# Performance work log

Hardware: AMD Instinct MI355X
Metric: run time of the kernel (lower is better)

The kernel has to match this reference:

```python
import jax, jax.numpy as jnp
import numpy as np

T, B, D_IN, H = 512, 64, 512, 1024


def setup_inputs() -> dict:
    key = jax.random.key(0)
    ks = jax.random.split(key, 6)
    s = 1.0 / np.sqrt(D_IN + H)  # torch Linear default init scale
    return {
        "x": jax.random.normal(ks[0], (T, B, D_IN), jnp.float32),
        "h0": jnp.zeros((B, H), jnp.float32),
        "C0": jnp.zeros((B, H), jnp.float32),
        "W_in": jax.random.normal(ks[1], (D_IN + H, H), jnp.float32) * s,
        "b_in": jnp.zeros((H,), jnp.float32),
        "W_over": jax.random.normal(ks[2], (D_IN + H, H), jnp.float32) * s,
        "b_over": jnp.zeros((H,), jnp.float32),
        "W_out": jax.random.normal(ks[3], (D_IN + H, H), jnp.float32) * s,
        "b_out": jnp.zeros((H,), jnp.float32),
        "W_intern": jax.random.normal(ks[4], (D_IN + H, H), jnp.float32) * s,
        "b_intern": jnp.zeros((H,), jnp.float32),
    }


def reference(x, h0, C0, W_in, b_in, W_over, b_over, W_out, b_out, W_intern, b_intern):
    # Faithful translation: concat order is (h, x) per one_step.
    def step(carry, xt):
        h, C = carry
        xc = jnp.concatenate([h, xt], axis=1)               # [B, H + D_IN]
        to_keep = jax.nn.sigmoid(xc @ W_in + b_in)          # input gate
        to_throw = jax.nn.sigmoid(xc @ W_over + b_over)     # forget gate
        out = jax.nn.sigmoid(xc @ W_out + b_out)            # output gate
        Ct = to_throw * C + to_keep * jnp.tanh(xc @ W_intern + b_intern)
        ht = out * jnp.tanh(Ct)
        return (ht, Ct), ht

    (hT, CT), hs = jax.lax.scan(step, (h0, C0), x)
    return hs, CT  # ([T, B, H], [B, H])
```

## Files before the change

### kernel.cpp

```cpp
#include <hip/hip_runtime.h>
#include <hip/hip_bf16.h>
#include <stdint.h>

#define T_STEPS 512
#define BATCH   64
#define DIN     512
#define HID     1024
#define KDIM    1536
#define NBLK    128
#define HPB     8
#define GCPB    32
#define KGRPS   192

typedef __bf16 bf16x8 __attribute__((ext_vector_type(8)));
typedef float  f32x4  __attribute__((ext_vector_type(4)));
typedef unsigned short ushort_t;
typedef unsigned long long u64_t;

__device__ __forceinline__ ushort_t f2bf(float f) {
    union { float f; unsigned u; } v; v.f = f;
    unsigned u = v.u;
    u += 0x7FFFu + ((u >> 16) & 1u);
    return (ushort_t)(u >> 16);
}

__device__ __forceinline__ float fast_sig(float x) {
    return __builtin_amdgcn_rcpf(1.0f + __expf(-x));
}
__device__ __forceinline__ float fast_tanh(float x) {
    float e = __expf(2.0f * x);
    return 1.0f - 2.0f * __builtin_amdgcn_rcpf(e + 1.0f);
}

__global__ void cvt_x(const float* __restrict__ x, ushort_t* __restrict__ xb, int n8) {
    int i = blockIdx.x * blockDim.x + threadIdx.x;
    if (i >= n8) return;
    float4 v0 = ((const float4*)x)[2 * i];
    float4 v1 = ((const float4*)x)[2 * i + 1];
    uint4 o;
    o.x = (unsigned)f2bf(v0.x) | ((unsigned)f2bf(v0.y) << 16);
    o.y = (unsigned)f2bf(v0.z) | ((unsigned)f2bf(v0.w) << 16);
    o.z = (unsigned)f2bf(v1.x) | ((unsigned)f2bf(v1.y) << 16);
    o.w = (unsigned)f2bf(v1.z) | ((unsigned)f2bf(v1.w) << 16);
    ((uint4*)xb)[i] = o;
}

__global__ void xpose_w(const float* __restrict__ Wi, const float* __restrict__ Wf,
                        const float* __restrict__ Wo, const float* __restrict__ Wg,
                        ushort_t* __restrict__ wt) {
    __shared__ float tile[64][65];
    int kt = blockIdx.x, nt = blockIdx.y, g = blockIdx.z;
    const float* W = (g == 0) ? Wi : (g == 1) ? Wf : (g == 2) ? Wo : Wg;
    int k0 = kt * 64, n0 = nt * 64;
    int c = threadIdx.x & 63, r0 = threadIdx.x >> 6;
#pragma unroll
    for (int i = 0; i < 16; ++i) {
        int r = r0 + i * 4;
        tile[r][c] = W[(size_t)(k0 + r) * HID + n0 + c];
    }
    __syncthreads();
#pragma unroll
    for (int p = 0; p < 2; ++p) {
        int q = threadIdx.x + p * 256;
        int n_inner = q & 7;
        int kgl = (q >> 3) & 7;
        int bl = q >> 6;
        int n = n0 + bl * 8 + n_inner;
        int blk = n >> 3;
        int nn = g * 8 + (n & 7);
        int kgrp = (k0 >> 3) + kgl;
        __align__(16) ushort_t tmp[8];
#pragma unroll
        for (int j = 0; j < 8; ++j) tmp[j] = f2bf(tile[kgl * 8 + j][bl * 8 + n_inner]);
        *(uint4*)(wt + ((((size_t)blk * KGRPS + kgrp) * GCPB + nn) << 3)) = *(const uint4*)tmp;
    }
}

__global__ __launch_bounds__(256, 1) void lstm_persist(
    const ushort_t* __restrict__ xbf,
    const ushort_t* __restrict__ wt,
    const float* __restrict__ h0, const float* __restrict__ C0,
    const float* __restrict__ b_i, const float* __restrict__ b_f,
    const float* __restrict__ b_o, const float* __restrict__ b_g,
    ushort_t* __restrict__ hbuf,
    unsigned* __restrict__ flags,
    float* __restrict__ out)
{
    __shared__ float gbuf[4][BATCH][GCPB + 2];
    __shared__ float Cl[BATCH][HPB + 1];
    __shared__ float biasl[GCPB];

    const int tid  = threadIdx.x;
    const int blk  = blockIdx.x;
    const int wave = tid >> 6;
    const int lane = tid & 63;
    const int j0   = blk * HPB;
    const int m_lane = lane & 15;
    const int quad   = lane >> 4;
    const int koff   = quad * 8;

    const ushort_t* wblk = wt + (size_t)blk * KGRPS * GCPB * 8;
    bf16x8 wbx[4][2], wbh[8][2];
#pragma unroll
    for (int cc = 0; cc < 4; ++cc) {
        const int kgrp = (32 + wave * 4 + cc) * 4 + quad;
        wbx[cc][0] = *(const bf16x8*)(wblk + ((size_t)kgrp * GCPB + m_lane) * 8);
        wbx[cc][1] = *(const bf16x8*)(wblk + ((size_t)kgrp * GCPB + 16 + m_lane) * 8);
    }
#pragma unroll
    for (int cc = 0; cc < 8; ++cc) {
        const int kgrp = (wave * 8 + cc) * 4 + quad;
        wbh[cc][0] = *(const bf16x8*)(wblk + ((size_t)kgrp * GCPB + m_lane) * 8);
        wbh[cc][1] = *(const bf16x8*)(wblk + ((size_t)kgrp * GCPB + 16 + m_lane) * 8);
    }

    if (tid < GCPB) {
        int g = tid >> 3, j = tid & 7;
        const float* bp = (g == 0) ? b_i : (g == 1) ? b_f : (g == 2) ? b_o : b_g;
        biasl[tid] = bp[j0 + j];
    }
    if (tid < 128) {
        int b = tid >> 1, jh = (tid & 1) * 4;
#pragma unroll
        for (int jj = 0; jj < 4; ++jj)
            Cl[b][jh + jj] = C0[b * HID + j0 + jh + jj];
        u64_t pk = 0;
#pragma unroll
        for (int jj = 0; jj < 4; ++jj)
            pk |= (u64_t)f2bf(h0[b * HID + j0 + jh + jj]) << (16 * jj);
        __hip_atomic_store((u64_t*)(hbuf + b * HID + j0 + jh), pk,
                           __ATOMIC_RELAXED, __HIP_MEMORY_SCOPE_AGENT);
    }
    asm volatile("s_waitcnt vmcnt(0)" ::: "memory");
    __syncthreads();
    if (tid == 0)
        __hip_atomic_store(&flags[blk * 32], 1u, __ATOMIC_RELAXED, __HIP_MEMORY_SCOPE_AGENT);

    int pb = 0;
    for (int t = 0; t < T_STEPS; ++t) {
        const ushort_t* xsrc = xbf + (size_t)t * BATCH * DIN;
        const ushort_t* hsrc = hbuf + pb * BATCH * HID;

        f32x4 acc[4][2];
#pragma unroll
        for (int rt = 0; rt < 4; ++rt)
#pragma unroll
            for (int ct = 0; ct < 2; ++ct)
                acc[rt][ct] = (f32x4){0.f, 0.f, 0.f, 0.f};

        bf16x8 ax[4][4];
#pragma unroll
        for (int cc = 0; cc < 4; ++cc) {
            const ushort_t* ap = xsrc + (wave * 4 + cc) * 32 + koff;
#pragma unroll
            for (int rt = 0; rt < 4; ++rt)
                ax[cc][rt] = *(const bf16x8*)(ap + (size_t)(rt * 16 + m_lane) * DIN);
        }
        __builtin_amdgcn_sched_barrier(0);

        if (tid < NBLK) {
            while (__hip_atomic_load(&flags[tid * 32], __ATOMIC_RELAXED,
                                     __HIP_MEMORY_SCOPE_AGENT) < (unsigned)(t + 1))
                __builtin_amdgcn_s_sleep(1);
        }
        __syncthreads();
        __builtin_amdgcn_fence(__ATOMIC_ACQUIRE, "agent");

        bf16x8 ah[8][4];
#pragma unroll
        for (int cc = 0; cc < 8; ++cc) {
            const ushort_t* ap = hsrc + (wave * 8 + cc) * 32 + koff;
#pragma unroll
            for (int rt = 0; rt < 4; ++rt)
                ah[cc][rt] = *(const bf16x8*)(ap + (size_t)(rt * 16 + m_lane) * HID);
        }
        __builtin_amdgcn_sched_barrier(0);

        asm volatile("" ::
            "v"(ax[0][0]), "v"(ax[0][1]), "v"(ax[0][2]), "v"(ax[0][3]),
            "v"(ax[1][0]), "v"(ax[1][1]), "v"(ax[1][2]), "v"(ax[1][3]),
            "v"(ax[2][0]), "v"(ax[2][1]), "v"(ax[2][2]), "v"(ax[2][3]),
            "v"(ax[3][0]), "v"(ax[3][1]), "v"(ax[3][2]), "v"(ax[3][3]));
#pragma unroll
        for (int cc = 0; cc < 4; ++cc)
#pragma unroll
            for (int rt = 0; rt < 4; ++rt) {
                acc[rt][0] = __builtin_amdgcn_mfma_f32_16x16x32_bf16(ax[cc][rt], wbx[cc][0], acc[rt][0], 0, 0, 0);
                acc[rt][1] = __builtin_amdgcn_mfma_f32_16x16x32_bf16(ax[cc][rt], wbx[cc][1], acc[rt][1], 0, 0, 0);
            }

        asm volatile("" ::
            "v"(ah[0][0]), "v"(ah[0][1]), "v"(ah[0][2]), "v"(ah[0][3]),
            "v"(ah[1][0]), "v"(ah[1][1]), "v"(ah[1][2]), "v"(ah[1][3]),
            "v"(ah[2][0]), "v"(ah[2][1]), "v"(ah[2][2]), "v"(ah[2][3]),
            "v"(ah[3][0]), "v"(ah[3][1]), "v"(ah[3][2]), "v"(ah[3][3]));
        asm volatile("" ::
            "v"(ah[4][0]), "v"(ah[4][1]), "v"(ah[4][2]), "v"(ah[4][3]),
            "v"(ah[5][0]), "v"(ah[5][1]), "v"(ah[5][2]), "v"(ah[5][3]),
            "v"(ah[6][0]), "v"(ah[6][1]), "v"(ah[6][2]), "v"(ah[6][3]),
            "v"(ah[7][0]), "v"(ah[7][1]), "v"(ah[7][2]), "v"(ah[7][3]));

#pragma unroll
        for (int cc = 0; cc < 8; ++cc)
#pragma unroll
            for (int rt = 0; rt < 4; ++rt) {
                acc[rt][0] = __builtin_amdgcn_mfma_f32_16x16x32_bf16(ah[cc][rt], wbh[cc][0], acc[rt][0], 0, 0, 0);
                acc[rt][1] = __builtin_amdgcn_mfma_f32_16x16x32_bf16(ah[cc][rt], wbh[cc][1], acc[rt][1], 0, 0, 0);
            }

#pragma unroll
        for (int rt = 0; rt < 4; ++rt)
#pragma unroll
            for (int ct = 0; ct < 2; ++ct)
#pragma unroll
                for (int r = 0; r < 4; ++r)
                    gbuf[wave][rt * 16 + quad * 4 + r][ct * 16 + m_lane] = acc[rt][ct][r];
        __syncthreads();

        float hv[4], cv[4];
        int b = tid >> 1, jh = (tid & 1) * 4;
        if (tid < 128) {
#pragma unroll
            for (int jj = 0; jj < 4; ++jj) {
                int j = jh + jj;
                float pre[4];
#pragma unroll
                for (int g = 0; g < 4; ++g) {
                    int col = g * 8 + j;
                    pre[g] = biasl[col] + gbuf[0][b][col] + gbuf[1][b][col]
                                        + gbuf[2][b][col] + gbuf[3][b][col];
                }
                float ig = fast_sig(pre[0]);
                float fg = fast_sig(pre[1]);
                float og = fast_sig(pre[2]);
                float gg = fast_tanh(pre[3]);
                float c_new = fg * Cl[b][jh + jj] + ig * gg;
                Cl[b][jh + jj] = c_new;
                cv[jj] = c_new;
                hv[jj] = og * fast_tanh(c_new);
            }
            u64_t pk = (u64_t)f2bf(hv[0]) | ((u64_t)f2bf(hv[1]) << 16)
                     | ((u64_t)f2bf(hv[2]) << 32) | ((u64_t)f2bf(hv[3]) << 48);
            __hip_atomic_store((u64_t*)(hbuf + (1 - pb) * BATCH * HID + b * HID + j0 + jh),
                               pk, __ATOMIC_RELAXED, __HIP_MEMORY_SCOPE_AGENT);
        }
        asm volatile("s_waitcnt vmcnt(0)" ::: "memory");
        __syncthreads();
        if (tid == 0)
            __hip_atomic_store(&flags[blk * 32], (unsigned)(t + 2), __ATOMIC_RELAXED,
                               __HIP_MEMORY_SCOPE_AGENT);

        if (tid < 128) {
            float4 o4; o4.x = hv[0]; o4.y = hv[1]; o4.z = hv[2]; o4.w = hv[3];
            *(float4*)(out + (size_t)t * BATCH * HID + b * HID + j0 + jh) = o4;
            if (t == T_STEPS - 1) {
                float4 c4; c4.x = cv[0]; c4.y = cv[1]; c4.z = cv[2]; c4.w = cv[3];
                *(float4*)(out + (size_t)T_STEPS * BATCH * HID + b * HID + j0 + jh) = c4;
            }
        }
        pb ^= 1;
    }
}

extern "C" void kernel_launch(void* const* d_in, const int* in_sizes, int n_in,
                              void* d_out, int out_size, void* d_ws, size_t ws_size,
                              hipStream_t stream) {
    (void)in_sizes; (void)n_in; (void)out_size; (void)ws_size;
    const float* x  = (const float*)d_in[0];
    const float* h0 = (const float*)d_in[1];
    const float* C0 = (const float*)d_in[2];
    const float* Wi = (const float*)d_in[3];
    const float* bi = (const float*)d_in[4];
    const float* Wf = (const float*)d_in[5];
    const float* bf = (const float*)d_in[6];
    const float* Wo = (const float*)d_in[7];
    const float* bo = (const float*)d_in[8];
    const float* Wg = (const float*)d_in[9];
    const float* bg = (const float*)d_in[10];
    float* out = (float*)d_out;

    char* ws = (char*)d_ws;
    unsigned*  flags = (unsigned*)ws;
    ushort_t*  hbuf  = (ushort_t*)(ws + 16384);
    ushort_t*  xb    = (ushort_t*)(ws + 16384 + 262144);
    ushort_t*  wt    = (ushort_t*)(ws + 16384 + 262144 + 33554432);

    hipMemsetAsync(flags, 0, 16384, stream);
    cvt_x<<<8192, 256, 0, stream>>>(x, xb, (T_STEPS * BATCH * DIN) / 8);
    xpose_w<<<dim3(24, 16, 4), 256, 0, stream>>>(Wi, Wf, Wo, Wg, wt);
    lstm_persist<<<NBLK, 256, 0, stream>>>(xb, wt, h0, C0, bi, bf, bo, bg, hbuf, flags, out);
}
```

Measured before the change: 5.381 ms.

## Halve persistent blocks to 64, widen per-block hidden slice, stage x-weights in LDS

The persistent LSTM kernel now runs 64 blocks, each owning 16 hidden units (64 gate columns) instead of 8, so fewer blocks take part in the per-step flag barrier. The recurrent-weight slice still lives in registers, now twice as wide. The input-weight slice has moved into a shared-memory buffer and is read back each step. All 256 threads now run the gate epilogue. The aim is to cut cross-block synchronisation and polling cost, in exchange for twice the MFMA work per block and extra LDS reads on the critical path.

Result: faster. 4.790 ms (-11.0%).

```diff
diff --git a/kernel.cpp b/kernel.cpp
--- a/kernel.cpp
+++ b/kernel.cpp
@@ -7,10 +7,11 @@
 #define DIN     512
 #define HID     1024
 #define KDIM    1536
-#define NBLK    128
-#define HPB     8
-#define GCPB    32
+#define NBLK    64
+#define HPB     16
+#define GCPB    64
 #define KGRPS   192
+#define XKG     64
 
 typedef __bf16 bf16x8 __attribute__((ext_vector_type(8)));
 typedef float  f32x4  __attribute__((ext_vector_type(4)));
@@ -66,8 +67,8 @@
         int kgl = (q >> 3) & 7;
         int bl = q >> 6;
         int n = n0 + bl * 8 + n_inner;
-        int blk = n >> 3;
-        int nn = g * 8 + (n & 7);
+        int blk = n >> 4;
+        int nn = g * HPB + (n & 15);
         int kgrp = (k0 >> 3) + kgl;
         __align__(16) ushort_t tmp[8];
 #pragma unroll
@@ -86,6 +87,7 @@
     unsigned* __restrict__ flags,
     float* __restrict__ out)
 {
+    __shared__ __align__(16) ushort_t Wlx[XKG][GCPB][8];
     __shared__ float gbuf[4][BATCH][GCPB + 2];
     __shared__ float Cl[BATCH][HPB + 1];
     __shared__ float biasl[GCPB];
@@ -100,27 +102,28 @@
     const int koff   = quad * 8;
 
     const ushort_t* wblk = wt + (size_t)blk * KGRPS * GCPB * 8;
-    bf16x8 wbx[4][2], wbh[8][2];
-#pragma unroll
-    for (int cc = 0; cc < 4; ++cc) {
-        const int kgrp = (32 + wave * 4 + cc) * 4 + quad;
-        wbx[cc][0] = *(const bf16x8*)(wblk + ((size_t)kgrp * GCPB + m_lane) * 8);
-        wbx[cc][1] = *(const bf16x8*)(wblk + ((size_t)kgrp * GCPB + 16 + m_lane) * 8);
-    }
+
+    bf16x8 wbh[8][4];
 #pragma unroll
     for (int cc = 0; cc < 8; ++cc) {
         const int kgrp = (wave * 8 + cc) * 4 + quad;
-        wbh[cc][0] = *(const bf16x8*)(wblk + ((size_t)kgrp * GCPB + m_lane) * 8);
-        wbh[cc][1] = *(const bf16x8*)(wblk + ((size_t)kgrp * GCPB + 16 + m_lane) * 8);
+#pragma unroll
+        for (int ct = 0; ct < 4; ++ct)
+            wbh[cc][ct] = *(const bf16x8*)(wblk + ((size_t)kgrp * GCPB + ct * 16 + m_lane) * 8);
+    }
+    {
+        const uint4* src = (const uint4*)(wblk + (size_t)128 * GCPB * 8);
+        uint4* dst = (uint4*)(&Wlx[0][0][0]);
+        for (int i = tid; i < XKG * GCPB; i += 256) dst[i] = src[i];
     }
 
     if (tid < GCPB) {
-        int g = tid >> 3, j = tid & 7;
+        int g = tid >> 4, j = tid & 15;
         const float* bp = (g == 0) ? b_i : (g == 1) ? b_f : (g == 2) ? b_o : b_g;
         biasl[tid] = bp[j0 + j];
     }
-    if (tid < 128) {
-        int b = tid >> 1, jh = (tid & 1) * 4;
+    {
+        int b = tid >> 2, jh = (tid & 3) * 4;
 #pragma unroll
         for (int jj = 0; jj < 4; ++jj)
             Cl[b][jh + jj] = C0[b * HID + j0 + jh + jj];
@@ -141,11 +144,11 @@
         const ushort_t* xsrc = xbf + (size_t)t * BATCH * DIN;
         const ushort_t* hsrc = hbuf + pb * BATCH * HID;
 
-        f32x4 acc[4][2];
+        f32x4 acc[4][4];
 #pragma unroll
         for (int rt = 0; rt < 4; ++rt)
 #pragma unroll
-            for (int ct = 0; ct < 2; ++ct)
+            for (int ct = 0; ct < 4; ++ct)
                 acc[rt][ct] = (f32x4){0.f, 0.f, 0.f, 0.f};
 
         bf16x8 ax[4][4];
@@ -165,6 +168,7 @@
         }
         __syncthreads();
         __builtin_amdgcn_fence(__ATOMIC_ACQUIRE, "agent");
+        __builtin_amdgcn_sched_barrier(0);
 
         bf16x8 ah[8][4];
 #pragma unroll
@@ -176,81 +180,69 @@
         }
         __builtin_amdgcn_sched_barrier(0);
 
-        asm volatile("" ::
-            "v"(ax[0][0]), "v"(ax[0][1]), "v"(ax[0][2]), "v"(ax[0][3]),
-            "v"(ax[1][0]), "v"(ax[1][1]), "v"(ax[1][2]), "v"(ax[1][3]),
-            "v"(ax[2][0]), "v"(ax[2][1]), "v"(ax[2][2]), "v"(ax[2][3]),
-            "v"(ax[3][0]), "v"(ax[3][1]), "v"(ax[3][2]), "v"(ax[3][3]));
-#pragma unroll
-        for (int cc = 0; cc < 4; ++cc)
-#pragma unroll
-            for (int rt = 0; rt < 4; ++rt) {
-                acc[rt][0] = __builtin_amdgcn_mfma_f32_16x16x32_bf16(ax[cc][rt], wbx[cc][0], acc[rt][0], 0, 0, 0);
-                acc[rt][1] = __builtin_amdgcn_mfma_f32_16x16x32_bf16(ax[cc][rt], wbx[cc][1], acc[rt][1], 0, 0, 0);
-            }
-
-        asm volatile("" ::
-            "v"(ah[0][0]), "v"(ah[0][1]), "v"(ah[0][2]), "v"(ah[0][3]),
-            "v"(ah[1][0]), "v"(ah[1][1]), "v"(ah[1][2]), "v"(ah[1][3]),
-            "v"(ah[2][0]), "v"(ah[2][1]), "v"(ah[2][2]), "v"(ah[2][3]),
-            "v"(ah[3][0]), "v"(ah[3][1]), "v"(ah[3][2]), "v"(ah[3][3]));
-        asm volatile("" ::
-            "v"(ah[4][0]), "v"(ah[4][1]), "v"(ah[4][2]), "v"(ah[4][3]),
-            "v"(ah[5][0]), "v"(ah[5][1]), "v"(ah[5][2]), "v"(ah[5][3]),
-            "v"(ah[6][0]), "v"(ah[6][1]), "v"(ah[6][2]), "v"(ah[6][3]),
-            "v"(ah[7][0]), "v"(ah[7][1]), "v"(ah[7][2]), "v"(ah[7][3]));
+#pragma unroll
+        for (int cc = 0; cc < 4; ++cc) {
+            const int kgx = (wave * 4 + cc) * 4 + quad;
+            bf16x8 bb[4];
+#pragma unroll
+            for (int ct = 0; ct < 4; ++ct)
+                bb[ct] = *(const bf16x8*)(&Wlx[kgx][ct * 16 + m_lane][0]);
+#pragma unroll
+            for (int rt = 0; rt < 4; ++rt)
+#pragma unroll
+                for (int ct = 0; ct < 4; ++ct)
+                    acc[rt][ct] = __builtin_amdgcn_mfma_f32_16x16x32_bf16(ax[cc][rt], bb[ct], acc[rt][ct], 0, 0, 0);
+        }
 
 #pragma unroll
         for (int cc = 0; cc < 8; ++cc)
 #pragma unroll
-            for (int rt = 0; rt < 4; ++rt) {
-                acc[rt][0] = __builtin_amdgcn_mfma_f32_16x16x32_bf16(ah[cc][rt], wbh[cc][0], acc[rt][0], 0, 0, 0);
-                acc[rt][1] = __builtin_amdgcn_mfma_f32_16x16x32_bf16(ah[cc][rt], wbh[cc][1], acc[rt][1], 0, 0, 0);
-            }
+            for (int rt = 0; rt < 4; ++rt)
+#pragma unroll
+                for (int ct = 0; ct < 4; ++ct)
+                    acc[rt][ct] = __builtin_amdgcn_mfma_f32_16x16x32_bf16(ah[cc][rt], wbh[cc][ct], acc[rt][ct], 0, 0, 0);
 
 #pragma unroll
         for (int rt = 0; rt < 4; ++rt)
 #pragma unroll
-            for (int ct = 0; ct < 2; ++ct)
+            for (int ct = 0; ct < 4; ++ct)
 #pragma unroll
                 for (int r = 0; r < 4; ++r)
                     gbuf[wave][rt * 16 + quad * 4 + r][ct * 16 + m_lane] = acc[rt][ct][r];
         __syncthreads();
 
         float hv[4], cv[4];
-        int b = tid >> 1, jh = (tid & 1) * 4;
-        if (tid < 128) {
-#pragma unroll
-            for (int jj = 0; jj < 4; ++jj) {
-                int j = jh + jj;
-                float pre[4];
-#pragma unroll
-                for (int g = 0; g < 4; ++g) {
-                    int col = g * 8 + j;
-                    pre[g] = biasl[col] + gbuf[0][b][col] + gbuf[1][b][col]
-                                        + gbuf[2][b][col] + gbuf[3][b][col];
-                }
-                float ig = fast_sig(pre[0]);
-                float fg = fast_sig(pre[1]);
-                float og = fast_sig(pre[2]);
-                float gg = fast_tanh(pre[3]);
-                float c_new = fg * Cl[b][jh + jj] + ig * gg;
-                Cl[b][jh + jj] = c_new;
-                cv[jj] = c_new;
-                hv[jj] = og * fast_tanh(c_new);
+        const int b = tid >> 2, jh = (tid & 3) * 4;
+#pragma unroll
+        for (int jj = 0; jj < 4; ++jj) {
+            int j = jh + jj;
+            float pre[4];
+#pragma unroll
+            for (int g = 0; g < 4; ++g) {
+                int col = g * HPB + j;
+                pre[g] = biasl[col] + gbuf[0][b][col] + gbuf[1][b][col]
+                                    + gbuf[2][b][col] + gbuf[3][b][col];
             }
-            u64_t pk = (u64_t)f2bf(hv[0]) | ((u64_t)f2bf(hv[1]) << 16)
-                     | ((u64_t)f2bf(hv[2]) << 32) | ((u64_t)f2bf(hv[3]) << 48);
-            __hip_atomic_store((u64_t*)(hbuf + (1 - pb) * BATCH * HID + b * HID + j0 + jh),
-                               pk, __ATOMIC_RELAXED, __HIP_MEMORY_SCOPE_AGENT);
-        }
+            float ig = fast_sig(pre[0]);
+            float fg = fast_sig(pre[1]);
+            float og = fast_sig(pre[2]);
+            float gg = fast_tanh(pre[3]);
+            float c_new = fg * Cl[b][jh + jj] + ig * gg;
+            Cl[b][jh + jj] = c_new;
+            cv[jj] = c_new;
+            hv[jj] = og * fast_tanh(c_new);
+        }
+        u64_t pk = (u64_t)f2bf(hv[0]) | ((u64_t)f2bf(hv[1]) << 16)
+                 | ((u64_t)f2bf(hv[2]) << 32) | ((u64_t)f2bf(hv[3]) << 48);
+        __hip_atomic_store((u64_t*)(hbuf + (1 - pb) * BATCH * HID + b * HID + j0 + jh),
+                           pk, __ATOMIC_RELAXED, __HIP_MEMORY_SCOPE_AGENT);
         asm volatile("s_waitcnt vmcnt(0)" ::: "memory");
         __syncthreads();
         if (tid == 0)
             __hip_atomic_store(&flags[blk * 32], (unsigned)(t + 2), __ATOMIC_RELAXED,
                                __HIP_MEMORY_SCOPE_AGENT);
 
-        if (tid < 128) {
+        {
             float4 o4; o4.x = hv[0]; o4.y = hv[1]; o4.z = hv[2]; o4.w = hv[3];
             *(float4*)(out + (size_t)t * BATCH * HID + b * HID + j0 + jh) = o4;
             if (t == T_STEPS - 1) {
```
